# Kernel optimization log

Measured on AMD Instinct MI355X. Metric: run time of the kernel, lower is better.

Reference implementation:

```python
import jax, jax.numpy as jnp
import numpy as np

B, T, H, CH = 8192, 10, 512, 512  # batch, time_step, hidden_size, code_hidden_size (must be equal)


def setup_inputs() -> dict:
    key = jax.random.key(0)
    ks = jax.random.split(key, 18)
    s = 0.05
    inp = {
        "h": jax.random.normal(ks[0], (B, T, CH), dtype=jnp.float32),
        "y_seq": jax.random.normal(ks[1], (B, T), dtype=jnp.float32),
        "attn1_w": jax.random.normal(ks[2], (CH, 2 * H), dtype=jnp.float32) * s,
        "attn1_b": jax.random.normal(ks[3], (CH,), dtype=jnp.float32) * s,
        "attn2_w": jax.random.normal(ks[4], (CH, CH), dtype=jnp.float32) * s,
        "attn2_b": jax.random.normal(ks[5], (CH,), dtype=jnp.float32) * s,
        "attn3_w": jax.random.normal(ks[6], (1, CH), dtype=jnp.float32) * s,
        "attn3_b": jax.random.normal(ks[7], (1,), dtype=jnp.float32) * s,
        "W_ih": jax.random.normal(ks[8], (4 * H, 1), dtype=jnp.float32) * s,
        "W_hh": jax.random.normal(ks[9], (4 * H, H), dtype=jnp.float32) * s,
        "b_ih": jax.random.normal(ks[10], (4 * H,), dtype=jnp.float32) * s,
        "b_hh": jax.random.normal(ks[11], (4 * H,), dtype=jnp.float32) * s,
        "fc1_w": jax.random.normal(ks[12], (H, CH + H), dtype=jnp.float32) * s,
        "fc1_b": jax.random.normal(ks[13], (H,), dtype=jnp.float32) * s,
        "fc2_w": jax.random.normal(ks[14], (1, H), dtype=jnp.float32) * s,
        "fc2_b": jax.random.normal(ks[15], (1,), dtype=jnp.float32) * s,
    }
    return inp


def reference(h, y_seq, attn1_w, attn1_b, attn2_w, attn2_b, attn3_w, attn3_b,
              W_ih, W_hh, b_ih, b_hh, fc1_w, fc1_b, fc2_w, fc2_b):
    # h: [B, T, CH] -> scan over time; y_seq: [B, T]
    h_t = jnp.transpose(h, (1, 0, 2))      # [T, B, CH]
    y_t = jnp.transpose(y_seq, (1, 0))     # [T, B]
    b = h.shape[0]
    hid = W_hh.shape[1]
    d0 = jnp.zeros((b, hid), dtype=h.dtype)
    s0 = jnp.zeros((b, hid), dtype=h.dtype)

    def step(carry, xs):
        d, s = carry
        ht, yt = xs  # ht: [B, CH], yt: [B]
        # attention scores (note: original softmax is over a singleton dim -> weights == 1)
        x = jnp.concatenate([d, ht], axis=1)                       # [B, 2H]
        a = jnp.tanh((x @ attn1_w.T + attn1_b) @ attn2_w.T + attn2_b)
        w = a @ attn3_w.T + attn3_b                                # [B, 1]
        w = jax.nn.softmax(w, axis=1)                              # softmax over size-1 dim == 1
        h1 = w * ht                                                # [B, H] (CH == H)
        # single LSTM step with h0 = h1, c0 = s, input = yt (scalar feature)
        gates = yt[:, None] @ W_ih.T + b_ih + h1 @ W_hh.T + b_hh   # [B, 4H]
        i, f, g, o = jnp.split(gates, 4, axis=1)
        c = jax.nn.sigmoid(f) * s + jax.nn.sigmoid(i) * jnp.tanh(g)
        d_new = jax.nn.sigmoid(o) * jnp.tanh(c)
        return (d_new, c), None

    (d, s), _ = jax.lax.scan(step, (d0, s0), (h_t, y_t))
    z = jnp.concatenate([d, h_t[-1]], axis=1)                      # [B, CH+H]
    y_res = (z @ fc1_w.T + fc1_b) @ fc2_w.T + fc2_b                # [B, 1]
    return y_res
```

## Files before the change

### kernel.cpp

```cpp
#include <hip/hip_runtime.h>
#include <stdint.h>

typedef __attribute__((ext_vector_type(8))) short short8;
typedef __attribute__((ext_vector_type(4))) float f32x4;
typedef unsigned short ushort_t;

#define T_STEPS 10
#define WPACK_BYTES (2048*1024)
#define VBUF_OFF  WPACK_BYTES
#define HBF_OFF   (WPACK_BYTES + 8192)
#define H_ELEMS   (8192ull*T_STEPS*512)
#define HBF_BYTES (H_ELEMS*2)

typedef const __attribute__((address_space(1))) void gas_void;
typedef __attribute__((address_space(3))) void las_void;

__device__ __forceinline__ void gld_lds16(const void* g, void* l){
  __builtin_amdgcn_global_load_lds((gas_void*)g, (las_void*)l, 16, 0, 0);
}

__device__ __forceinline__ unsigned int pk2(float x, float y){
  unsigned int bx = __float_as_uint(x), by = __float_as_uint(y);
  bx = (bx + 0x7FFFu + ((bx>>16)&1u)) >> 16;
  by = (by + 0x7FFFu + ((by>>16)&1u)) >> 16;
  return bx | (by<<16);
}
__device__ __forceinline__ float sigf(float x){ return 1.f/(1.f + __expf(-x)); }
__device__ __forceinline__ float tanh_(float x){
  x = fminf(fmaxf(x, -15.f), 15.f);
  float e = __expf(2.f*x);
  return (e - 1.f)/(e + 1.f);
}

__global__ __launch_bounds__(256) void k_pack(const float* __restrict__ Whh,
                                              ushort_t* __restrict__ wp){
  int id  = blockIdx.x*256 + threadIdx.x;
  int row = id >> 6;
  int ko  = (id & 63) * 8;
  const float* p = Whh + row*512 + ko;
  float4 a = *(const float4*)p, b = *(const float4*)(p+4);
  uint4 v;
  v.x = pk2(a.x,a.y); v.y = pk2(a.z,a.w);
  v.z = pk2(b.x,b.y); v.w = pk2(b.z,b.w);
  int g = row >> 9, j = row & 511;
  int jb = j >> 6, jt = (j >> 4) & 3, jl = j & 15;
  int kc = ko >> 5, khi = (ko >> 3) & 3, lane = khi*16 + jl;
  int chunk = ((jb*4 + jt)*4 + g)*16 + kc;
  *(uint4*)(wp + chunk*512 + lane*8) = v;
}

__global__ __launch_bounds__(256) void k_v(const float* __restrict__ fc1w,
                                           const float* __restrict__ fc1b,
                                           const float* __restrict__ fc2w,
                                           const float* __restrict__ fc2b,
                                           float* __restrict__ vout,
                                           float* __restrict__ bias0){
  __shared__ float red[4][64];
  int tid = threadIdx.x;
  if (blockIdx.x < 16){
    int j  = blockIdx.x*64 + (tid & 63);
    int hc = tid >> 6;
    float s = 0.f;
    for (int hh = hc*128; hh < hc*128 + 128; ++hh)
      s += fc2w[hh] * fc1w[hh*1024 + j];
    red[hc][tid & 63] = s;
    __syncthreads();
    if (tid < 64)
      vout[blockIdx.x*64 + tid] = red[0][tid]+red[1][tid]+red[2][tid]+red[3][tid];
  } else {
    if (tid < 64){
      float s = 0.f;
      for (int i = 0; i < 8; ++i){ int hh = i*64 + tid; s += fc2w[hh]*fc1b[hh]; }
      for (int m = 32; m; m >>= 1) s += __shfl_xor(s, m);
      if (tid == 0) *bias0 = s + fc2b[0];
    }
  }
}

__global__ __launch_bounds__(512) void k_init(const float* __restrict__ h,
                                              const float* __restrict__ v,
                                              const float* __restrict__ bias0,
                                              float* __restrict__ out){
  int w = threadIdx.x >> 6, lane = threadIdx.x & 63;
  float b0v = *bias0;
  const float* v2 = v + 512;
  for (int r = 0; r < 8; ++r){
    int b = blockIdx.x*64 + w*8 + r;
    const float* hp = h + ((size_t)b*T_STEPS + 9)*512 + lane*8;
    float4 x0 = *(const float4*)hp, x1 = *(const float4*)(hp+4);
    const float* vp = v2 + lane*8;
    float4 w0 = *(const float4*)vp, w1 = *(const float4*)(vp+4);
    float s = x0.x*w0.x + x0.y*w0.y + x0.z*w0.z + x0.w*w0.w
            + x1.x*w1.x + x1.y*w1.y + x1.z*w1.z + x1.w*w1.w;
    for (int m = 32; m; m >>= 1) s += __shfl_xor(s, m);
    if (lane == 0) out[b] = s + b0v;
  }
}

__global__ __launch_bounds__(256) void k_prep(const float* __restrict__ h,
                                              ushort_t* __restrict__ hbf){
  __shared__ __align__(16) ushort_t buf[8192*8];
  int bid = blockIdx.x;
  int T = bid / 20, rem = bid % 20, t = rem >> 1, half = rem & 1;
  int tid = threadIdx.x;
  int row128 = tid >> 1, khalf = tid & 1;
  const float* src = h + ((size_t)(T*256 + half*128 + row128)*T_STEPS + t)*512
                   + khalf*256;
#pragma unroll
  for (int g = 0; g < 32; ++g){
    int k0 = khalf*256 + g*8;
    float4 a = *(const float4*)(src + g*8);
    float4 b = *(const float4*)(src + g*8 + 4);
    uint4 pk;
    pk.x = pk2(a.x,a.y); pk.y = pk2(a.z,a.w);
    pk.z = pk2(b.x,b.y); pk.w = pk2(b.z,b.w);
    int kc = k0 >> 5, kq = (k0 >> 3) & 3;
    *(uint4*)&buf[(size_t)(kc*512 + kq*128 + row128)*8] = pk;
  }
  __syncthreads();
  size_t sb = ((size_t)(T*T_STEPS + t)*16)*1024;
#pragma unroll
  for (int i = 0; i < 32; ++i){
    int gr = tid + i*256;
    int kc = gr >> 9, kq = (gr >> 7) & 3, r = gr & 127;
    size_t dg = sb + (size_t)kc*1024 + kq*256 + half*128 + r;
    *(uint4*)(hbf + dg*8) = *(const uint4*)&buf[gr*8];
  }
}

__global__ __launch_bounds__(512)
__attribute__((amdgpu_waves_per_eu(2, 2)))
void k_main_p(const ushort_t* __restrict__ hbf, const float* __restrict__ y,
              const float* __restrict__ Wih, const float* __restrict__ bih,
              const float* __restrict__ bhh,
              const ushort_t* __restrict__ wpack, const float* __restrict__ v1,
              float* __restrict__ out)
{
  __shared__ __align__(16) ushort_t Wlds[96*512];
  __shared__ float ys[256*T_STEPS];

  int tid = threadIdx.x;
  int w = tid >> 6, lane = tid & 63, lhi = lane >> 4, llo = lane & 15;
  int bid = blockIdx.x;
  int xcd = bid & 7, q = bid >> 3;
  int jb  = q & 15;
  int tile = xcd*4 + (q >> 4);
  int b0 = tile * 256;

  float bias2[4][2], wihv[4][2], v1v[2];
#pragma unroll
  for (int g = 0; g < 4; ++g)
#pragma unroll
    for (int n = 0; n < 2; ++n){
      int col = g*512 + jb*32 + n*16 + llo;
      bias2[g][n] = bih[col] + bhh[col];
      wihv[g][n]  = Wih[col];
    }
#pragma unroll
  for (int n = 0; n < 2; ++n) v1v[n] = v1[jb*32 + n*16 + llo];

  for (int i = tid; i < 256*T_STEPS; i += 512)
    ys[i] = y[(size_t)b0*T_STEPS + i];

#pragma unroll
  for (int i = 0; i < 12; ++i){
    int c = w*12 + i;
    int g = c >> 5, n = (c >> 4) & 1, kc = c & 15;
    int ch = (((jb >> 1)*4 + ((jb & 1)*2 + n))*4 + g)*16 + kc;
    gld_lds16(wpack + (size_t)ch*512 + lane*8, Wlds + c*512);
  }
  __syncthreads();

  const ushort_t* wl = Wlds + lane*8;
  const ushort_t* aT = hbf + (size_t)tile*1310720
                     + (size_t)(lhi*256 + w*32 + llo)*8;

  f32x4 acc[2][3][2];
  float cst[2][2][4];
#pragma unroll
  for (int m = 0; m < 2; ++m)
#pragma unroll
    for (int n = 0; n < 2; ++n){
#pragma unroll
      for (int g = 0; g < 3; ++g) acc[m][g][n] = (f32x4){0.f,0.f,0.f,0.f};
#pragma unroll
      for (int r = 0; r < 4; ++r) cst[m][n][r] = 0.f;
    }

#pragma unroll 1
  for (int t = 0; t < T_STEPS; ++t){
    const ushort_t* ap = aT;
    short8 afA[2], wfA[3][2], afB[2], wfB[3][2];
#pragma unroll
    for (int m = 0; m < 2; ++m) afA[m] = *(const short8*)(ap + m*128);
#pragma unroll
    for (int g = 0; g < 3; ++g)
#pragma unroll
      for (int n = 0; n < 2; ++n)
        wfA[g][n] = *(const short8*)(wl + (g*2+n)*8192);

#pragma unroll 1
    for (int kp = 0; kp < 8; ++kp){
      const ushort_t* wk1 = wl + (2*kp + 1)*512;
#pragma unroll
      for (int m = 0; m < 2; ++m) afB[m] = *(const short8*)(ap + 8192 + m*128);
#pragma unroll
      for (int g = 0; g < 3; ++g)
#pragma unroll
        for (int n = 0; n < 2; ++n)
          wfB[g][n] = *(const short8*)(wk1 + (g*2+n)*8192);
#pragma unroll
      for (int g = 0; g < 3; ++g)
#pragma unroll
        for (int n = 0; n < 2; ++n)
#pragma unroll
          for (int m = 0; m < 2; ++m)
            acc[m][g][n] = __builtin_amdgcn_mfma_f32_16x16x32_bf16(
                afA[m], wfA[g][n], acc[m][g][n], 0, 0, 0);
      if (kp < 7){
        const ushort_t* wk2 = wl + (2*kp + 2)*512;
#pragma unroll
        for (int m = 0; m < 2; ++m) afA[m] = *(const short8*)(ap + 16384 + m*128);
#pragma unroll
        for (int g = 0; g < 3; ++g)
#pragma unroll
          for (int n = 0; n < 2; ++n)
            wfA[g][n] = *(const short8*)(wk2 + (g*2+n)*8192);
      }
#pragma unroll
      for (int g = 0; g < 3; ++g)
#pragma unroll
        for (int n = 0; n < 2; ++n)
#pragma unroll
          for (int m = 0; m < 2; ++m)
            acc[m][g][n] = __builtin_amdgcn_mfma_f32_16x16x32_bf16(
                afB[m], wfB[g][n], acc[m][g][n], 0, 0, 0);
      ap += 16384;
    }

#pragma unroll
    for (int m = 0; m < 2; ++m)
#pragma unroll
      for (int r = 0; r < 4; ++r){
        float yr = ys[(w*32 + m*16 + lhi*4 + r)*T_STEPS + t];
#pragma unroll
        for (int n = 0; n < 2; ++n){
          float pi = acc[m][0][n][r] + fmaf(yr, wihv[0][n], bias2[0][n]);
          float pf = acc[m][1][n][r] + fmaf(yr, wihv[1][n], bias2[1][n]);
          float pg = acc[m][2][n][r] + fmaf(yr, wihv[2][n], bias2[2][n]);
          cst[m][n][r] = sigf(pf)*cst[m][n][r] + sigf(pi)*tanh_(pg);
        }
      }
#pragma unroll
    for (int m = 0; m < 2; ++m)
#pragma unroll
      for (int g = 0; g < 3; ++g)
#pragma unroll
        for (int n = 0; n < 2; ++n) acc[m][g][n] = (f32x4){0.f,0.f,0.f,0.f};

    aT += 131072;
  }

  f32x4 acco[2][2];
#pragma unroll
  for (int m = 0; m < 2; ++m)
#pragma unroll
    for (int n = 0; n < 2; ++n) acco[m][n] = (f32x4){0.f,0.f,0.f,0.f};

  {
    const ushort_t* ap = aT - 131072;
    const ushort_t* wo0 = wpack + (size_t)((((jb>>1)*4 + (jb&1)*2 + 0)*4 + 3)*16)*512 + lane*8;
    const ushort_t* wo1 = wpack + (size_t)((((jb>>1)*4 + (jb&1)*2 + 1)*4 + 3)*16)*512 + lane*8;
    short8 afA[2], woA[2], afB[2], woB[2];
#pragma unroll
    for (int m = 0; m < 2; ++m) afA[m] = *(const short8*)(ap + m*128);
    woA[0] = *(const short8*)(wo0);
    woA[1] = *(const short8*)(wo1);

#pragma unroll 1
    for (int kp = 0; kp < 8; ++kp){
#pragma unroll
      for (int m = 0; m < 2; ++m) afB[m] = *(const short8*)(ap + 8192 + m*128);
      woB[0] = *(const short8*)(wo0 + (2*kp+1)*512);
      woB[1] = *(const short8*)(wo1 + (2*kp+1)*512);
#pragma unroll
      for (int n = 0; n < 2; ++n)
#pragma unroll
        for (int m = 0; m < 2; ++m)
          acco[m][n] = __builtin_amdgcn_mfma_f32_16x16x32_bf16(
              afA[m], woA[n], acco[m][n], 0, 0, 0);
      if (kp < 7){
#pragma unroll
        for (int m = 0; m < 2; ++m) afA[m] = *(const short8*)(ap + 16384 + m*128);
        woA[0] = *(const short8*)(wo0 + (2*kp+2)*512);
        woA[1] = *(const short8*)(wo1 + (2*kp+2)*512);
      }
#pragma unroll
      for (int n = 0; n < 2; ++n)
#pragma unroll
        for (int m = 0; m < 2; ++m)
          acco[m][n] = __builtin_amdgcn_mfma_f32_16x16x32_bf16(
              afB[m], woB[n], acco[m][n], 0, 0, 0);
      ap += 16384;
    }
  }

#pragma unroll
  for (int m = 0; m < 2; ++m)
#pragma unroll
    for (int r = 0; r < 4; ++r){
      float yr = ys[(w*32 + m*16 + lhi*4 + r)*T_STEPS + 9];
      float val = 0.f;
#pragma unroll
      for (int n = 0; n < 2; ++n){
        float po = acco[m][n][r] + fmaf(yr, wihv[3][n], bias2[3][n]);
        val += sigf(po)*tanh_(cst[m][n][r])*v1v[n];
      }
      val += __shfl_xor(val, 1);
      val += __shfl_xor(val, 2);
      val += __shfl_xor(val, 4);
      val += __shfl_xor(val, 8);
      if (llo == 0)
        atomicAdd(&out[b0 + w*32 + m*16 + lhi*4 + r], val);
    }
}

__global__ __launch_bounds__(256)
__attribute__((amdgpu_waves_per_eu(2, 2)))
void k_main_f(const float* __restrict__ h, const float* __restrict__ y,
              const float* __restrict__ Wih, const float* __restrict__ bih,
              const float* __restrict__ bhh,
              const ushort_t* __restrict__ wpack, const float* __restrict__ v1,
              float* __restrict__ out)
{
  __shared__ __align__(16) ushort_t Abf[2][4096];
  __shared__ float ysf[128*T_STEPS];

  int tid = threadIdx.x;
  int w = tid >> 6, lane = tid & 63, lhi = lane >> 4, llo = lane & 15;
  int mh = w & 1, wj = w >> 1;
  int bid = blockIdx.x;
  int xcd = bid & 7, q = bid >> 3;
  int jb = q >> 3, tile = xcd*8 + (q & 7);
  int b0 = tile * 128;

  float bias2[4][2], wihv[4][2], v1v[2];
#pragma unroll
  for (int g = 0; g < 4; ++g)
#pragma unroll
    for (int n = 0; n < 2; ++n){
      int col = g*512 + jb*64 + (wj*2+n)*16 + llo;
      bias2[g][n] = bih[col] + bhh[col];
      wihv[g][n]  = Wih[col];
    }
#pragma unroll
  for (int n = 0; n < 2; ++n) v1v[n] = v1[jb*64 + (wj*2+n)*16 + llo];

  for (int i = tid; i < 128*T_STEPS; i += 256)
    ysf[i] = y[(size_t)b0*T_STEPS + i];

  const ushort_t* wbase = wpack + (size_t)(jb*4 + wj*2)*32768 + lane*8;

  auto stageA_f = [&](int parity, int ss){
    int t = (ss < 160) ? (ss >> 4) : 9;
    int kc = ss & 15;
#pragma unroll
    for (int i = 0; i < 2; ++i){
      int gidx = tid + i*256;
      int kq = gidx >> 7, row = gidx & 127;
      const float* p = h + ((size_t)(b0+row)*T_STEPS + t)*512 + kc*32 + kq*8;
      float4 x0 = *(const float4*)p, x1 = *(const float4*)(p+4);
      uint4 pk;
      pk.x = pk2(x0.x,x0.y); pk.y = pk2(x0.z,x0.w);
      pk.z = pk2(x1.x,x1.y); pk.w = pk2(x1.z,x1.w);
      *(uint4*)&Abf[parity][gidx*8] = pk;
    }
  };

  stageA_f(0, 0);
  __syncthreads();

  f32x4 acc[4][3][2];
  float cst[4][2][4];
#pragma unroll
  for (int m = 0; m < 4; ++m)
#pragma unroll
    for (int n = 0; n < 2; ++n){
#pragma unroll
      for (int g = 0; g < 3; ++g) acc[m][g][n] = (f32x4){0.f,0.f,0.f,0.f};
#pragma unroll
      for (int r = 0; r < 4; ++r) cst[m][n][r] = 0.f;
    }

  const int aro = (lhi*128 + mh*64 + llo)*8;

#pragma unroll 1
  for (int s = 0; s < 160; ++s){
    if (s < 159) stageA_f((s+1)&1, s+1);
    else         stageA_f(0, 160);

    int kco = (s & 15) * 512;
    short8 wf[3][2];
#pragma unroll
    for (int g = 0; g < 3; ++g)
#pragma unroll
      for (int n = 0; n < 2; ++n)
        wf[g][n] = *(const short8*)(wbase + (size_t)(n*4+g)*8192 + kco);

    const ushort_t* ap = &Abf[s&1][aro];
    short8 af[4];
#pragma unroll
    for (int m = 0; m < 4; ++m)
      af[m] = *(const short8*)(ap + m*128);

#pragma unroll
    for (int g = 0; g < 3; ++g)
#pragma unroll
      for (int n = 0; n < 2; ++n)
#pragma unroll
        for (int m = 0; m < 4; ++m)
          acc[m][g][n] = __builtin_amdgcn_mfma_f32_16x16x32_bf16(
              af[m], wf[g][n], acc[m][g][n], 0, 0, 0);

    if ((s & 15) == 15){
      int t = s >> 4;
#pragma unroll
      for (int m = 0; m < 4; ++m)
#pragma unroll
        for (int r = 0; r < 4; ++r){
          float yr = ysf[(mh*64 + m*16 + lhi*4 + r)*T_STEPS + t];
#pragma unroll
          for (int n = 0; n < 2; ++n){
            float pi = acc[m][0][n][r] + fmaf(yr, wihv[0][n], bias2[0][n]);
            float pf = acc[m][1][n][r] + fmaf(yr, wihv[1][n], bias2[1][n]);
            float pg = acc[m][2][n][r] + fmaf(yr, wihv[2][n], bias2[2][n]);
            cst[m][n][r] = sigf(pf)*cst[m][n][r] + sigf(pi)*tanh_(pg);
          }
        }
#pragma unroll
      for (int m = 0; m < 4; ++m)
#pragma unroll
        for (int g = 0; g < 3; ++g)
#pragma unroll
          for (int n = 0; n < 2; ++n) acc[m][g][n] = (f32x4){0.f,0.f,0.f,0.f};
    }
    __syncthreads();
  }

  f32x4 acco[4][2];
#pragma unroll
  for (int m = 0; m < 4; ++m)
#pragma unroll
    for (int n = 0; n < 2; ++n) acco[m][n] = (f32x4){0.f,0.f,0.f,0.f};

#pragma unroll 1
  for (int s2 = 0; s2 < 16; ++s2){
    if (s2 < 15) stageA_f((s2+1)&1, 161+s2);
    int kco = s2 * 512;
    short8 wo[2];
#pragma unroll
    for (int n = 0; n < 2; ++n)
      wo[n] = *(const short8*)(wbase + (size_t)(n*4+3)*8192 + kco);

    const ushort_t* ap = &Abf[s2&1][aro];
    short8 af[4];
#pragma unroll
    for (int m = 0; m < 4; ++m)
      af[m] = *(const short8*)(ap + m*128);
#pragma unroll
    for (int n = 0; n < 2; ++n)
#pragma unroll
      for (int m = 0; m < 4; ++m)
        acco[m][n] = __builtin_amdgcn_mfma_f32_16x16x32_bf16(
            af[m], wo[n], acco[m][n], 0, 0, 0);
    __syncthreads();
  }

#pragma unroll
  for (int m = 0; m < 4; ++m)
#pragma unroll
    for (int r = 0; r < 4; ++r){
      float yr = ysf[(mh*64 + m*16 + lhi*4 + r)*T_STEPS + 9];
      float val = 0.f;
#pragma unroll
      for (int n = 0; n < 2; ++n){
        float po = acco[m][n][r] + fmaf(yr, wihv[3][n], bias2[3][n]);
        val += sigf(po)*tanh_(cst[m][n][r])*v1v[n];
      }
      val += __shfl_xor(val, 1);
      val += __shfl_xor(val, 2);
      val += __shfl_xor(val, 4);
      val += __shfl_xor(val, 8);
      if (llo == 0)
        atomicAdd(&out[b0 + mh*64 + m*16 + lhi*4 + r], val);
    }
}

extern "C" void kernel_launch(void* const* d_in, const int* in_sizes, int n_in,
                              void* d_out, int out_size, void* d_ws, size_t ws_size,
                              hipStream_t stream){
  (void)in_sizes; (void)n_in; (void)out_size;
  const float* h    = (const float*)d_in[0];
  const float* y    = (const float*)d_in[1];
  const float* Wih  = (const float*)d_in[8];
  const float* Whh  = (const float*)d_in[9];
  const float* bih  = (const float*)d_in[10];
  const float* bhh  = (const float*)d_in[11];
  const float* fc1w = (const float*)d_in[12];
  const float* fc1b = (const float*)d_in[13];
  const float* fc2w = (const float*)d_in[14];
  const float* fc2b = (const float*)d_in[15];
  float* out = (float*)d_out;

  ushort_t* wpack = (ushort_t*)d_ws;
  float* vbuf  = (float*)((char*)d_ws + VBUF_OFF);
  float* bias0 = vbuf + 1024;
  ushort_t* hbf = (ushort_t*)((char*)d_ws + HBF_OFF);
  bool prep = ws_size >= (size_t)HBF_OFF + HBF_BYTES;

  k_pack<<<512, 256, 0, stream>>>(Whh, wpack);
  k_v<<<17, 256, 0, stream>>>(fc1w, fc1b, fc2w, fc2b, vbuf, bias0);
  if (prep)
    k_prep<<<640, 256, 0, stream>>>(h, hbf);
  k_init<<<128, 512, 0, stream>>>(h, vbuf, bias0, out);
  if (prep)
    k_main_p<<<512, 512, 0, stream>>>(hbf, y, Wih, bih, bhh, wpack, vbuf, out);
  else
    k_main_f<<<512, 256, 0, stream>>>(h, y, Wih, bih, bhh, wpack, vbuf, out);
}
```

Measured before the change: 231.4 us.

## Halve per-block hidden-column tile to double grid and occupancy in main kernel

Each block of the prepped main kernel now covers 16 hidden columns instead of 32, so it holds half the weight slice in LDS and half the accumulators. The grid doubles to 1024 blocks and the waves-per-EU hint is raised to 4, aiming for more resident waves to hide global load latency on the streamed h operand. The cost is that every A-fragment of h is now loaded twice as often across blocks, doubling h traffic from L2/HBM and halving MFMA work per A load.

```diff
diff --git a/kernel.cpp b/kernel.cpp
--- a/kernel.cpp
+++ b/kernel.cpp
@@ -129,44 +129,41 @@
 }
 
 __global__ __launch_bounds__(512)
-__attribute__((amdgpu_waves_per_eu(2, 2)))
+__attribute__((amdgpu_waves_per_eu(4)))
 void k_main_p(const ushort_t* __restrict__ hbf, const float* __restrict__ y,
               const float* __restrict__ Wih, const float* __restrict__ bih,
               const float* __restrict__ bhh,
               const ushort_t* __restrict__ wpack, const float* __restrict__ v1,
               float* __restrict__ out)
 {
-  __shared__ __align__(16) ushort_t Wlds[96*512];
+  __shared__ __align__(16) ushort_t Wlds[48*512];
   __shared__ float ys[256*T_STEPS];
 
   int tid = threadIdx.x;
   int w = tid >> 6, lane = tid & 63, lhi = lane >> 4, llo = lane & 15;
   int bid = blockIdx.x;
   int xcd = bid & 7, q = bid >> 3;
-  int jb  = q & 15;
-  int tile = xcd*4 + (q >> 4);
+  int jb  = q & 31;
+  int tile = xcd*4 + (q >> 5);
   int b0 = tile * 256;
 
-  float bias2[4][2], wihv[4][2], v1v[2];
-#pragma unroll
-  for (int g = 0; g < 4; ++g)
-#pragma unroll
-    for (int n = 0; n < 2; ++n){
-      int col = g*512 + jb*32 + n*16 + llo;
-      bias2[g][n] = bih[col] + bhh[col];
-      wihv[g][n]  = Wih[col];
-    }
-#pragma unroll
-  for (int n = 0; n < 2; ++n) v1v[n] = v1[jb*32 + n*16 + llo];
+  float bias2[4], wihv[4];
+#pragma unroll
+  for (int g = 0; g < 4; ++g){
+    int col = g*512 + jb*16 + llo;
+    bias2[g] = bih[col] + bhh[col];
+    wihv[g]  = Wih[col];
+  }
+  float v1v = v1[jb*16 + llo];
 
   for (int i = tid; i < 256*T_STEPS; i += 512)
     ys[i] = y[(size_t)b0*T_STEPS + i];
 
 #pragma unroll
-  for (int i = 0; i < 12; ++i){
-    int c = w*12 + i;
-    int g = c >> 5, n = (c >> 4) & 1, kc = c & 15;
-    int ch = (((jb >> 1)*4 + ((jb & 1)*2 + n))*4 + g)*16 + kc;
+  for (int i = 0; i < 6; ++i){
+    int c = w*6 + i;
+    int g = c >> 4, kc = c & 15;
+    int ch = (jb*4 + g)*16 + kc;
     gld_lds16(wpack + (size_t)ch*512 + lane*8, Wlds + c*512);
   }
   __syncthreads();
@@ -175,29 +172,25 @@
   const ushort_t* aT = hbf + (size_t)tile*1310720
                      + (size_t)(lhi*256 + w*32 + llo)*8;
 
-  f32x4 acc[2][3][2];
-  float cst[2][2][4];
-#pragma unroll
-  for (int m = 0; m < 2; ++m)
-#pragma unroll
-    for (int n = 0; n < 2; ++n){
-#pragma unroll
-      for (int g = 0; g < 3; ++g) acc[m][g][n] = (f32x4){0.f,0.f,0.f,0.f};
-#pragma unroll
-      for (int r = 0; r < 4; ++r) cst[m][n][r] = 0.f;
-    }
+  f32x4 acc[2][3];
+  float cst[2][4];
+#pragma unroll
+  for (int m = 0; m < 2; ++m){
+#pragma unroll
+    for (int g = 0; g < 3; ++g) acc[m][g] = (f32x4){0.f,0.f,0.f,0.f};
+#pragma unroll
+    for (int r = 0; r < 4; ++r) cst[m][r] = 0.f;
+  }
 
 #pragma unroll 1
   for (int t = 0; t < T_STEPS; ++t){
     const ushort_t* ap = aT;
-    short8 afA[2], wfA[3][2], afB[2], wfB[3][2];
+    short8 afA[2], wfA[3], afB[2], wfB[3];
 #pragma unroll
     for (int m = 0; m < 2; ++m) afA[m] = *(const short8*)(ap + m*128);
 #pragma unroll
     for (int g = 0; g < 3; ++g)
-#pragma unroll
-      for (int n = 0; n < 2; ++n)
-        wfA[g][n] = *(const short8*)(wl + (g*2+n)*8192);
+      wfA[g] = *(const short8*)(wl + g*8192);
 
 #pragma unroll 1
     for (int kp = 0; kp < 8; ++kp){
@@ -206,35 +199,27 @@
       for (int m = 0; m < 2; ++m) afB[m] = *(const short8*)(ap + 8192 + m*128);
 #pragma unroll
       for (int g = 0; g < 3; ++g)
-#pragma unroll
-        for (int n = 0; n < 2; ++n)
-          wfB[g][n] = *(const short8*)(wk1 + (g*2+n)*8192);
+        wfB[g] = *(const short8*)(wk1 + g*8192);
 #pragma unroll
       for (int g = 0; g < 3; ++g)
 #pragma unroll
-        for (int n = 0; n < 2; ++n)
-#pragma unroll
-          for (int m = 0; m < 2; ++m)
-            acc[m][g][n] = __builtin_amdgcn_mfma_f32_16x16x32_bf16(
-                afA[m], wfA[g][n], acc[m][g][n], 0, 0, 0);
+        for (int m = 0; m < 2; ++m)
+          acc[m][g] = __builtin_amdgcn_mfma_f32_16x16x32_bf16(
+              afA[m], wfA[g], acc[m][g], 0, 0, 0);
       if (kp < 7){
         const ushort_t* wk2 = wl + (2*kp + 2)*512;
 #pragma unroll
         for (int m = 0; m < 2; ++m) afA[m] = *(const short8*)(ap + 16384 + m*128);
 #pragma unroll
         for (int g = 0; g < 3; ++g)
-#pragma unroll
-          for (int n = 0; n < 2; ++n)
-            wfA[g][n] = *(const short8*)(wk2 + (g*2+n)*8192);
+          wfA[g] = *(const short8*)(wk2 + g*8192);
       }
 #pragma unroll
       for (int g = 0; g < 3; ++g)
 #pragma unroll
-        for (int n = 0; n < 2; ++n)
-#pragma unroll
-          for (int m = 0; m < 2; ++m)
-            acc[m][g][n] = __builtin_amdgcn_mfma_f32_16x16x32_bf16(
-                afB[m], wfB[g][n], acc[m][g][n], 0, 0, 0);
+        for (int m = 0; m < 2; ++m)
+          acc[m][g] = __builtin_amdgcn_mfma_f32_16x16x32_bf16(
+              afB[m], wfB[g], acc[m][g], 0, 0, 0);
       ap += 16384;
     }
 
@@ -243,64 +228,49 @@
 #pragma unroll
       for (int r = 0; r < 4; ++r){
         float yr = ys[(w*32 + m*16 + lhi*4 + r)*T_STEPS + t];
-#pragma unroll
-        for (int n = 0; n < 2; ++n){
-          float pi = acc[m][0][n][r] + fmaf(yr, wihv[0][n], bias2[0][n]);
-          float pf = acc[m][1][n][r] + fmaf(yr, wihv[1][n], bias2[1][n]);
-          float pg = acc[m][2][n][r] + fmaf(yr, wihv[2][n], bias2[2][n]);
-          cst[m][n][r] = sigf(pf)*cst[m][n][r] + sigf(pi)*tanh_(pg);
-        }
+        float pi = acc[m][0][r] + fmaf(yr, wihv[0], bias2[0]);
+        float pf = acc[m][1][r] + fmaf(yr, wihv[1], bias2[1]);
+        float pg = acc[m][2][r] + fmaf(yr, wihv[2], bias2[2]);
+        cst[m][r] = sigf(pf)*cst[m][r] + sigf(pi)*tanh_(pg);
       }
 #pragma unroll
     for (int m = 0; m < 2; ++m)
 #pragma unroll
-      for (int g = 0; g < 3; ++g)
-#pragma unroll
-        for (int n = 0; n < 2; ++n) acc[m][g][n] = (f32x4){0.f,0.f,0.f,0.f};
+      for (int g = 0; g < 3; ++g) acc[m][g] = (f32x4){0.f,0.f,0.f,0.f};
 
     aT += 131072;
   }
 
-  f32x4 acco[2][2];
-#pragma unroll
-  for (int m = 0; m < 2; ++m)
-#pragma unroll
-    for (int n = 0; n < 2; ++n) acco[m][n] = (f32x4){0.f,0.f,0.f,0.f};
+  f32x4 acco[2];
+#pragma unroll
+  for (int m = 0; m < 2; ++m) acco[m] = (f32x4){0.f,0.f,0.f,0.f};
 
   {
     const ushort_t* ap = aT - 131072;
-    const ushort_t* wo0 = wpack + (size_t)((((jb>>1)*4 + (jb&1)*2 + 0)*4 + 3)*16)*512 + lane*8;
-    const ushort_t* wo1 = wpack + (size_t)((((jb>>1)*4 + (jb&1)*2 + 1)*4 + 3)*16)*512 + lane*8;
-    short8 afA[2], woA[2], afB[2], woB[2];
+    const ushort_t* wo = wpack + (size_t)((jb*4 + 3)*16)*512 + lane*8;
+    short8 afA[2], woA, afB[2], woB;
 #pragma unroll
     for (int m = 0; m < 2; ++m) afA[m] = *(const short8*)(ap + m*128);
-    woA[0] = *(const short8*)(wo0);
-    woA[1] = *(const short8*)(wo1);
+    woA = *(const short8*)(wo);
 
 #pragma unroll 1
     for (int kp = 0; kp < 8; ++kp){
 #pragma unroll
       for (int m = 0; m < 2; ++m) afB[m] = *(const short8*)(ap + 8192 + m*128);
-      woB[0] = *(const short8*)(wo0 + (2*kp+1)*512);
-      woB[1] = *(const short8*)(wo1 + (2*kp+1)*512);
-#pragma unroll
-      for (int n = 0; n < 2; ++n)
-#pragma unroll
-        for (int m = 0; m < 2; ++m)
-          acco[m][n] = __builtin_amdgcn_mfma_f32_16x16x32_bf16(
-              afA[m], woA[n], acco[m][n], 0, 0, 0);
+      woB = *(const short8*)(wo + (2*kp+1)*512);
+#pragma unroll
+      for (int m = 0; m < 2; ++m)
+        acco[m] = __builtin_amdgcn_mfma_f32_16x16x32_bf16(
+            afA[m], woA, acco[m], 0, 0, 0);
       if (kp < 7){
 #pragma unroll
         for (int m = 0; m < 2; ++m) afA[m] = *(const short8*)(ap + 16384 + m*128);
-        woA[0] = *(const short8*)(wo0 + (2*kp+2)*512);
-        woA[1] = *(const short8*)(wo1 + (2*kp+2)*512);
+        woA = *(const short8*)(wo + (2*kp+2)*512);
       }
 #pragma unroll
-      for (int n = 0; n < 2; ++n)
-#pragma unroll
-        for (int m = 0; m < 2; ++m)
-          acco[m][n] = __builtin_amdgcn_mfma_f32_16x16x32_bf16(
-              afB[m], woB[n], acco[m][n], 0, 0, 0);
+      for (int m = 0; m < 2; ++m)
+        acco[m] = __builtin_amdgcn_mfma_f32_16x16x32_bf16(
+            afB[m], woB, acco[m], 0, 0, 0);
       ap += 16384;
     }
   }
@@ -310,12 +280,8 @@
 #pragma unroll
     for (int r = 0; r < 4; ++r){
       float yr = ys[(w*32 + m*16 + lhi*4 + r)*T_STEPS + 9];
-      float val = 0.f;
-#pragma unroll
-      for (int n = 0; n < 2; ++n){
-        float po = acco[m][n][r] + fmaf(yr, wihv[3][n], bias2[3][n]);
-        val += sigf(po)*tanh_(cst[m][n][r])*v1v[n];
-      }
+      float po = acco[m][r] + fmaf(yr, wihv[3], bias2[3]);
+      float val = sigf(po)*tanh_(cst[m][r])*v1v;
       val += __shfl_xor(val, 1);
       val += __shfl_xor(val, 2);
       val += __shfl_xor(val, 4);
@@ -326,7 +292,7 @@
 }
 
 __global__ __launch_bounds__(256)
-__attribute__((amdgpu_waves_per_eu(2, 2)))
+__attribute__((amdgpu_waves_per_eu(2)))
 void k_main_f(const float* __restrict__ h, const float* __restrict__ y,
               const float* __restrict__ Wih, const float* __restrict__ bih,
               const float* __restrict__ bhh,
@@ -524,7 +490,7 @@
     k_prep<<<640, 256, 0, stream>>>(h, hbf);
   k_init<<<128, 512, 0, stream>>>(h, vbuf, bias0, out);
   if (prep)
-    k_main_p<<<512, 512, 0, stream>>>(hbf, y, Wih, bih, bhh, wpack, vbuf, out);
+    k_main_p<<<1024, 512, 0, stream>>>(hbf, y, Wih, bih, bhh, wpack, vbuf, out);
   else
     k_main_f<<<512, 256, 0, stream>>>(h, y, Wih, bih, bhh, wpack, vbuf, out);
 }
```

Measured after the change: 246.9 us. 6.7% more time.
